# Performance work log

Measured on AMD Instinct MI355X. Metric: run time of the kernel, lower is better.

## Reference

```python
import jax, jax.numpy as jnp
import numpy as np

B, L, W = 4096, 30, 5          # batch, MAX_TOKEN_LENGTH, WINDOW_SIZE
A, E = 30, 128                 # ALPHABET_SIZE, embedding dim
C = 40                         # OUT_CHANNELS
H, T = 128, 3                  # LSTM_UNITS, num CRF tags
LIN = W * C                    # 200
EPS = 1e-5


def setup_inputs():
    key = jax.random.key(0)
    ks = jax.random.split(key, 24)
    def rn(k, shape, s=0.1):
        return jax.random.normal(k, shape, jnp.float32) * s
    return {
        'x': jax.random.randint(ks[0], (B, L, W), 0, A, jnp.int32),
        'emb': rn(ks[1], (A, E), 1.0),
        'conv_w': rn(ks[2], (C, E, 3)),
        'conv_b': rn(ks[3], (C,)),
        'bn1_g': 1.0 + rn(ks[4], (C,)),
        'bn1_b': rn(ks[5], (C,)),
        'bn1_m': rn(ks[6], (C,)),
        'bn1_v': 0.5 + jax.random.uniform(ks[7], (C,), jnp.float32),
        'w_ih_f': rn(ks[8], (4 * H, LIN)),
        'w_hh_f': rn(ks[9], (4 * H, H)),
        'b_f': rn(ks[10], (4 * H,)),
        'w_ih_b': rn(ks[11], (4 * H, LIN)),
        'w_hh_b': rn(ks[12], (4 * H, H)),
        'b_b': rn(ks[13], (4 * H,)),
        'bn2_g': 1.0 + rn(ks[14], (2 * H,)),
        'bn2_b': rn(ks[15], (2 * H,)),
        'bn2_m': rn(ks[16], (2 * H,)),
        'bn2_v': 0.5 + jax.random.uniform(ks[17], (2 * H,), jnp.float32),
        'fc_w': rn(ks[18], (T, 2 * H)),
        'fc_b': rn(ks[19], (T,)),
        'trans': rn(ks[20], (T, T)),
        'start_t': rn(ks[21], (T,)),
        'end_t': rn(ks[22], (T,)),
    }


def _lstm_dir(seq, w_ih, w_hh, b, reverse):
    # seq: [B, L, F]; torch gate order i, f, g, o
    xs = jnp.einsum('blf,gf->lbg', seq, w_ih) + b  # [L, B, 4H]
    h0 = jnp.zeros((seq.shape[0], H), seq.dtype)
    def step(carry, xt):
        h, c = carry
        z = xt + h @ w_hh.T
        i, f, g, o = jnp.split(z, 4, axis=-1)
        c = jax.nn.sigmoid(f) * c + jax.nn.sigmoid(i) * jnp.tanh(g)
        h = jax.nn.sigmoid(o) * jnp.tanh(c)
        return (h, c), h
    _, hs = jax.lax.scan(step, (h0, h0), xs, reverse=reverse)
    return hs.transpose(1, 0, 2)  # [B, L, H]


def _viterbi(emis, mask, trans, start_t, end_t):
    # emis: [B, L, T], mask: [B, L] bool
    score = start_t + emis[:, 0]                      # [B, T]
    def step(score, inp):
        e_t, m_t = inp                                # [B, T], [B]
        cand = score[:, :, None] + trans              # [B, Tprev, Tnext]
        ptr = jnp.argmax(cand, axis=1)                # [B, T]
        new = jnp.max(cand, axis=1) + e_t
        return jnp.where(m_t[:, None], new, score), ptr
    score, hist = jax.lax.scan(
        step, score, (emis[:, 1:].transpose(1, 0, 2), mask[:, 1:].T))
    score = score + end_t
    best = jnp.max(score, axis=1)                     # [B] path scores
    last = jnp.argmax(score, axis=1)                  # [B]
    def back(tag, inp):
        h_t, m_t = inp
        prev = jnp.take_along_axis(h_t, tag[:, None], axis=1)[:, 0]
        tag = jnp.where(m_t, prev, tag)
        return tag, tag
    _, ys = jax.lax.scan(back, last, (hist, mask[:, 1:].T), reverse=True)
    tags = jnp.concatenate([ys, last[None]], axis=0).T  # [B, L]
    return best, tags


def reference(x, emb, conv_w, conv_b, bn1_g, bn1_b, bn1_m, bn1_v,
              w_ih_f, w_hh_f, b_f, w_ih_b, w_hh_b, b_b,
              bn2_g, bn2_b, bn2_m, bn2_v, fc_w, fc_b, trans, start_t, end_t):
    mask = x[:, :, 2] > 0                             # [B, L]
    e = emb[x.reshape(B * L, W)]                      # [N, W, E]  (dropout=eval noop)
    e = e.transpose(0, 2, 1)                          # [N, E, W]
    y = jax.lax.conv_general_dilated(
        e, conv_w, (1,), [(1, 1)],
        dimension_numbers=('NCH', 'OIH', 'NCH')) + conv_b[:, None]
    # BatchNorm1d (inference, running stats)
    y = (y - bn1_m[:, None]) * (bn1_g / jnp.sqrt(bn1_v + EPS))[:, None] + bn1_b[:, None]
    y = jax.nn.relu(y)
    # MaxPool1d(k=3, stride=1, pad=1): length preserved
    y = jax.lax.reduce_window(y, -jnp.inf, jax.lax.max,
                              (1, 1, 3), (1, 1, 1),
                              [(0, 0), (0, 0), (1, 1)])
    y = y.reshape(B, L, LIN)                          # torch.flatten is channel-major = row-major reshape
    hf = _lstm_dir(y, w_ih_f, w_hh_f, b_f, False)
    hb = _lstm_dir(y, w_ih_b, w_hh_b, b_b, True)
    h = jnp.concatenate([hf, hb], axis=-1)            # [B, L, 2H]
    h = (h - bn2_m) * (bn2_g / jnp.sqrt(bn2_v + EPS)) + bn2_b
    emis = h @ fc_w.T + fc_b                          # [B, L, T]
    return _viterbi(emis, mask, trans, start_t, end_t)
```

## Files before the change

kernel.cpp:

```cpp
#include <hip/hip_runtime.h>
#include <math.h>

#define BB    4096
#define LL    30
#define WW    5
#define CC    40
#define HH    128
#define TT    3
#define KA    328
#define NB    32
#define NT_   512
#define FSTR  232
#define HSTR  136
#define CW    1056

#define WS_P    0
#define WS_BC   3600
#define WS_BG   3648
#define WS_WFC  4672
#define WS_EB   5440
#define WS_WBF  5504
#define WS_EMIS (5504 + 540672)

typedef __bf16 bf16x8 __attribute__((ext_vector_type(8)));
typedef float  f32x4  __attribute__((ext_vector_type(4)));
typedef unsigned short u16x8 __attribute__((ext_vector_type(8)));

__device__ __forceinline__ float sigm(float x) {
    return __builtin_amdgcn_rcpf(1.0f + __expf(-x));
}
__device__ __forceinline__ float tanh_fast(float x) {
    return 2.0f * __builtin_amdgcn_rcpf(1.0f + __expf(-2.0f * x)) - 1.0f;
}
__device__ __forceinline__ unsigned short f2bf(float f) {
    unsigned u = __builtin_bit_cast(unsigned, f);
    return (unsigned short)((u + 0x7FFFu + ((u >> 16) & 1u)) >> 16);
}
__device__ __forceinline__ float bf2f(unsigned short h) {
    unsigned u = ((unsigned)h) << 16;
    return __builtin_bit_cast(float, u);
}

__global__ void prep_kernel(const float* __restrict__ emb, const float* __restrict__ conv_w,
                            const float* __restrict__ conv_b,
                            const float* __restrict__ bn1_g, const float* __restrict__ bn1_b,
                            const float* __restrict__ bn1_m, const float* __restrict__ bn1_v,
                            const float* __restrict__ w_ih_f, const float* __restrict__ w_hh_f,
                            const float* __restrict__ b_f,
                            const float* __restrict__ w_ih_b, const float* __restrict__ w_hh_b,
                            const float* __restrict__ b_b,
                            const float* __restrict__ bn2_g, const float* __restrict__ bn2_b,
                            const float* __restrict__ bn2_m, const float* __restrict__ bn2_v,
                            const float* __restrict__ fc_w, const float* __restrict__ fc_b,
                            float* __restrict__ ws)
{
    const int gid = blockIdx.x * blockDim.x + threadIdx.x;
    const int gsz = gridDim.x * blockDim.x;

    for (int idx = gid; idx < 3600; idx += gsz) {
        int k = idx / 1200, rem = idx % 1200, a = rem / 40, c = rem % 40;
        float s1 = bn1_g[c] / sqrtf(bn1_v[c] + 1e-5f);
        float acc = 0.f;
        for (int e = 0; e < 128; ++e)
            acc += emb[a * 128 + e] * conv_w[(c * 128 + e) * 3 + k];
        ws[WS_P + idx] = acc * s1;
    }
    for (int c = gid; c < CC; c += gsz) {
        float s1 = bn1_g[c] / sqrtf(bn1_v[c] + 1e-5f);
        ws[WS_BC + c] = (conv_b[c] - bn1_m[c]) * s1 + bn1_b[c];
    }
    for (int i = gid; i < 1024; i += gsz) {
        int d = i >> 9, g = i & 511;
        ws[WS_BG + i] = d ? b_b[g] : b_f[g];
    }
    for (int i = gid; i < 768; i += gsz) {
        int d = i / 384, r = i % 384, t = r / 128, u = r % 128;
        int j = d * 128 + u;
        float s2 = bn2_g[j] / sqrtf(bn2_v[j] + 1e-5f);
        ws[WS_WFC + i] = fc_w[t * 256 + j] * s2;
    }
    for (int t = gid; t < TT; t += gsz) {
        float acc = fc_b[t];
        for (int j = 0; j < 256; ++j) {
            float s2 = bn2_g[j] / sqrtf(bn2_v[j] + 1e-5f);
            acc += fc_w[t * 256 + j] * (bn2_b[j] - bn2_m[j] * s2);
        }
        ws[WS_EB + t] = acc;
    }
    unsigned short* wsu = (unsigned short*)ws;
    for (int i = gid; i < 2 * 512 * CW; i += gsz) {
        int d = i / (512 * CW), r = i % (512 * CW);
        int n = r / CW, q = r % CW;
        int Ks = q / 96, t = q % 96, s = t / 32, k32 = t % 32;
        int k = Ks * 32 + k32;
        int u = n >> 2, g = n & 3, row = g * 128 + u;
        const float* wih = d ? w_ih_b : w_ih_f;
        const float* whh = d ? w_hh_b : w_hh_f;
        float w = (k < 200) ? wih[row * 200 + k]
                            : ((k >= 224) ? whh[row * 128 + (k - 224)] : 0.f);
        unsigned short t0 = f2bf(w);
        float r1 = w - bf2f(t0);
        unsigned short t1 = f2bf(r1);
        unsigned short t2 = f2bf(r1 - bf2f(t1));
        wsu[2 * WS_WBF + i] = (s == 0) ? t0 : ((s == 1) ? t1 : t2);
    }
}

__global__ __launch_bounds__(512, 2)
void lstm_kernel(const int* __restrict__ x, float* __restrict__ ws)
{
    __shared__ unsigned short Fh[2][NB * FSTR], Fl[2][NB * FSTR], Fm[2][NB * FSTR];
    __shared__ unsigned short Hh[2][NB * HSTR], Hl[2][NB * HSTR], Hm[2][NB * HSTR];
    __shared__ float Pp_s[3600];
    __shared__ float Wfc_s[384];
    __shared__ float biasC_s[40];

    const int tid = threadIdx.x;
    const int d   = blockIdx.x & 1;
    const int b0  = (blockIdx.x >> 1) * NB;

    const unsigned short* __restrict__ Wb =
        (const unsigned short*)ws + 2 * WS_WBF + d * (512 * CW);
    float* emis = ws + WS_EMIS + d * (BB * LL * TT);

    for (int i = tid; i < 3600; i += NT_) Pp_s[i] = ws[WS_P + i];
    for (int i = tid; i < 384;  i += NT_) Wfc_s[i] = ws[WS_WFC + d * 384 + i];
    for (int i = tid; i < 40;   i += NT_) biasC_s[i] = ws[WS_BC + i];
    for (int i = tid; i < NB * FSTR; i += NT_) {
        ((unsigned*)Fh)[i] = 0u; ((unsigned*)Fl)[i] = 0u; ((unsigned*)Fm)[i] = 0u;
    }
    for (int i = tid; i < NB * HSTR; i += NT_) {
        ((unsigned*)Hh)[i] = 0u; ((unsigned*)Hl)[i] = 0u; ((unsigned*)Hm)[i] = 0u;
    }

    const int lane = tid & 63;
    const int wv   = tid >> 6;
    const int quad = lane >> 4;
    const int ml   = lane & 15;

    const unsigned short* __restrict__ Wn[4] = {
        Wb + (wv * 64 +  0 + ml) * CW + quad * 8,
        Wb + (wv * 64 + 16 + ml) * CW + quad * 8,
        Wb + (wv * 64 + 32 + ml) * CW + quad * 8,
        Wb + (wv * 64 + 48 + ml) * CW + quad * 8
    };

    const float* bgp = ws + WS_BG + d * 512;
    int   un[4];
    float bIv[4], bFv[4], bGv[4], bOv[4];
    #pragma unroll
    for (int nt = 0; nt < 4; ++nt) {
        int u = wv * 16 + nt * 4 + quad;
        un[nt]  = u;
        bIv[nt] = bgp[u];
        bFv[nt] = bgp[128 + u];
        bGv[nt] = bgp[256 + u];
        bOv[nt] = bgp[384 + u];
    }

    float cst[2][4];
    #pragma unroll
    for (int mt = 0; mt < 2; ++mt)
        #pragma unroll
        for (int nt = 0; nt < 4; ++nt) cst[mt][nt] = 0.f;

    __syncthreads();

#define FEAT_ONE(LPOS, BUF, P)                                                 \
    {                                                                          \
        int bb = (P) / CC, c = (P) % CC;                                       \
        const int* tok = x + (((b0 + bb) * LL) + (LPOS)) * WW;                 \
        int t0 = tok[0], t1 = tok[1], t2 = tok[2], t3 = tok[3], t4 = tok[4];   \
        float bc = biasC_s[c];                                                 \
        float a0 = bc + Pp_s[(30 + t0) * 40 + c] + Pp_s[(60 + t1) * 40 + c];   \
        float a1 = bc + Pp_s[t0 * 40 + c] + Pp_s[(30 + t1) * 40 + c] + Pp_s[(60 + t2) * 40 + c]; \
        float a2 = bc + Pp_s[t1 * 40 + c] + Pp_s[(30 + t2) * 40 + c] + Pp_s[(60 + t3) * 40 + c]; \
        float a3 = bc + Pp_s[t2 * 40 + c] + Pp_s[(30 + t3) * 40 + c] + Pp_s[(60 + t4) * 40 + c]; \
        float a4 = bc + Pp_s[t3 * 40 + c] + Pp_s[(30 + t4) * 40 + c];          \
        a0 = fmaxf(a0, 0.f); a1 = fmaxf(a1, 0.f); a2 = fmaxf(a2, 0.f);         \
        a3 = fmaxf(a3, 0.f); a4 = fmaxf(a4, 0.f);                              \
        float f[5];                                                            \
        f[0] = fmaxf(a0, a1);                                                  \
        f[1] = fmaxf(fmaxf(a0, a1), a2);                                       \
        f[2] = fmaxf(fmaxf(a1, a2), a3);                                       \
        f[3] = fmaxf(fmaxf(a2, a3), a4);                                       \
        f[4] = fmaxf(a3, a4);                                                  \
        int base = bb * FSTR + c * 5;                                          \
        _Pragma("unroll")                                                      \
        for (int j = 0; j < 5; ++j) {                                          \
            unsigned short h0 = f2bf(f[j]);                                    \
            float r1 = f[j] - bf2f(h0);                                        \
            unsigned short h1 = f2bf(r1);                                      \
            unsigned short h2 = f2bf(r1 - bf2f(h1));                           \
            Fh[BUF][base + j] = h0;                                            \
            Fl[BUF][base + j] = h1;                                            \
            Fm[BUF][base + j] = h2;                                            \
        }                                                                      \
    }

#define FEAT_ALL(LPOS, BUF)                                                    \
    {                                                                          \
        FEAT_ONE(LPOS, BUF, tid)                                               \
        FEAT_ONE(LPOS, BUF, tid + 512)                                         \
        if (tid >= 256) FEAT_ONE(LPOS, BUF, tid + 768)                         \
    }

#define EMIS_BODY(LPOS, HB)                                                    \
    {                                                                          \
        int bb = tid / 6, r6 = tid % 6, t = r6 >> 1, seg = r6 & 1;             \
        int hoff = bb * HSTR + seg * 64;                                       \
        const float* wfc = &Wfc_s[t * 128 + seg * 64];                         \
        float s = 0.f;                                                         \
        _Pragma("unroll")                                                      \
        for (int i = 0; i < 8; ++i) {                                          \
            u16x8 v0 = *(const u16x8*)&Hh[HB][hoff + i * 8];                   \
            u16x8 v1 = *(const u16x8*)&Hl[HB][hoff + i * 8];                   \
            u16x8 v2 = *(const u16x8*)&Hm[HB][hoff + i * 8];                   \
            _Pragma("unroll")                                                  \
            for (int j = 0; j < 8; ++j) {                                      \
                float h = bf2f(v0[j]) + bf2f(v1[j]) + bf2f(v2[j]);             \
                s += h * wfc[i * 8 + j];                                       \
            }                                                                  \
        }                                                                      \
        s += __shfl_xor(s, 1);                                                 \
        if (seg == 0)                                                          \
            emis[(((b0 + bb) * LL) + (LPOS)) * TT + t] = s;                    \
    }

    {
        const int l0 = d ? (LL - 1) : 0;
        FEAT_ALL(l0, 0)
    }

#define WLOAD(B, P, KS)                                                        \
        {                                                                      \
            B[0] = *(const bf16x8*)((P) + (KS) * 96);                          \
            B[1] = *(const bf16x8*)((P) + (KS) * 96 + 32);                     \
            B[2] = *(const bf16x8*)((P) + (KS) * 96 + 64);                     \
        }
#define LDA(BUF, KS)                                                           \
        {                                                                      \
            if ((KS) < 7) {                                                    \
                const int ko_ = (KS) * 32 + quad * 8;                          \
                ah[BUF][0] = *(const bf16x8*)&Fh[fb][ml * FSTR + ko_];         \
                al[BUF][0] = *(const bf16x8*)&Fl[fb][ml * FSTR + ko_];         \
                am[BUF][0] = *(const bf16x8*)&Fm[fb][ml * FSTR + ko_];         \
                ah[BUF][1] = *(const bf16x8*)&Fh[fb][(16 + ml) * FSTR + ko_];  \
                al[BUF][1] = *(const bf16x8*)&Fl[fb][(16 + ml) * FSTR + ko_];  \
                am[BUF][1] = *(const bf16x8*)&Fm[fb][(16 + ml) * FSTR + ko_];  \
            } else {                                                           \
                const int ko_ = ((KS) - 7) * 32 + quad * 8;                    \
                ah[BUF][0] = *(const bf16x8*)&Hh[hr][ml * HSTR + ko_];         \
                al[BUF][0] = *(const bf16x8*)&Hl[hr][ml * HSTR + ko_];         \
                am[BUF][0] = *(const bf16x8*)&Hm[hr][ml * HSTR + ko_];         \
                ah[BUF][1] = *(const bf16x8*)&Hh[hr][(16 + ml) * HSTR + ko_];  \
                al[BUF][1] = *(const bf16x8*)&Hl[hr][(16 + ml) * HSTR + ko_];  \
                am[BUF][1] = *(const bf16x8*)&Hm[hr][(16 + ml) * HSTR + ko_];  \
            }                                                                  \
        }
#define GEMM6X(B, CB, NT)                                                      \
        {                                                                      \
            acc[0][NT] = __builtin_amdgcn_mfma_f32_16x16x32_bf16(B[0], ah[CB][0], acc[0][NT], 0, 0, 0); \
            acc[0][NT] = __builtin_amdgcn_mfma_f32_16x16x32_bf16(B[0], al[CB][0], acc[0][NT], 0, 0, 0); \
            acc[0][NT] = __builtin_amdgcn_mfma_f32_16x16x32_bf16(B[1], ah[CB][0], acc[0][NT], 0, 0, 0); \
            acc[0][NT] = __builtin_amdgcn_mfma_f32_16x16x32_bf16(B[1], al[CB][0], acc[0][NT], 0, 0, 0); \
            acc[0][NT] = __builtin_amdgcn_mfma_f32_16x16x32_bf16(B[2], ah[CB][0], acc[0][NT], 0, 0, 0); \
            acc[0][NT] = __builtin_amdgcn_mfma_f32_16x16x32_bf16(B[0], am[CB][0], acc[0][NT], 0, 0, 0); \
            acc[1][NT] = __builtin_amdgcn_mfma_f32_16x16x32_bf16(B[0], ah[CB][1], acc[1][NT], 0, 0, 0); \
            acc[1][NT] = __builtin_amdgcn_mfma_f32_16x16x32_bf16(B[0], al[CB][1], acc[1][NT], 0, 0, 0); \
            acc[1][NT] = __builtin_amdgcn_mfma_f32_16x16x32_bf16(B[1], ah[CB][1], acc[1][NT], 0, 0, 0); \
            acc[1][NT] = __builtin_amdgcn_mfma_f32_16x16x32_bf16(B[1], al[CB][1], acc[1][NT], 0, 0, 0); \
            acc[1][NT] = __builtin_amdgcn_mfma_f32_16x16x32_bf16(B[2], ah[CB][1], acc[1][NT], 0, 0, 0); \
            acc[1][NT] = __builtin_amdgcn_mfma_f32_16x16x32_bf16(B[0], am[CB][1], acc[1][NT], 0, 0, 0); \
        }

    bf16x8 wX[2][3], wY[2][3];
    WLOAD(wX[0], Wn[0], 0)
    WLOAD(wX[1], Wn[1], 0)

    __syncthreads();

    for (int step = 0; step < LL; ++step) {
        const int fb = step & 1;
        const int hw = step & 1;
        const int hr = hw ^ 1;

        f32x4 acc[2][4];
        #pragma unroll
        for (int mt = 0; mt < 2; ++mt)
            #pragma unroll
            for (int nt = 0; nt < 4; ++nt)
                acc[mt][nt] = (f32x4){0.f, 0.f, 0.f, 0.f};

        {
            bf16x8 ah[2][2], al[2][2], am[2][2];
            LDA(0, 0)

            #pragma unroll
            for (int Ks = 0; Ks < 11; ++Ks) {
                const int cb = Ks & 1, nb = cb ^ 1;

                WLOAD(wY[0], Wn[2], Ks)
                WLOAD(wY[1], Wn[3], Ks)
                if (Ks < 10) LDA(nb, Ks + 1)

                __builtin_amdgcn_s_setprio(1);
                GEMM6X(wX[0], cb, 0)
                GEMM6X(wX[1], cb, 1)
                __builtin_amdgcn_s_setprio(0);

                if (Ks < 10) {
                    WLOAD(wX[0], Wn[0], Ks + 1)
                    WLOAD(wX[1], Wn[1], Ks + 1)
                }
                __builtin_amdgcn_s_setprio(1);
                GEMM6X(wY[0], cb, 2)
                GEMM6X(wY[1], cb, 3)
                __builtin_amdgcn_s_setprio(0);

                if (Ks == 4 && step + 1 < LL && (wv & 1) == 0) {
                    const int lnext = d ? (LL - 2 - step) : (step + 1);
                    FEAT_ALL(lnext, fb ^ 1)
                }
                if (Ks == 8 && step + 1 < LL && (wv & 1) == 1) {
                    const int lnext = d ? (LL - 2 - step) : (step + 1);
                    FEAT_ALL(lnext, fb ^ 1)
                }
            }
        }

        if (step > 0 && tid < 192) {
            const int lprev = d ? (LL - step) : (step - 1);
            EMIS_BODY(lprev, hr)
        }

        #pragma unroll
        for (int mt = 0; mt < 2; ++mt) {
            #pragma unroll
            for (int nt = 0; nt < 4; ++nt) {
                float zi = acc[mt][nt][0] + bIv[nt];
                float zf = acc[mt][nt][1] + bFv[nt];
                float zg = acc[mt][nt][2] + bGv[nt];
                float zo = acc[mt][nt][3] + bOv[nt];
                float cn = sigm(zf) * cst[mt][nt] + sigm(zi) * tanh_fast(zg);
                cst[mt][nt] = cn;
                float h = sigm(zo) * tanh_fast(cn);
                unsigned short h0 = f2bf(h);
                float r1 = h - bf2f(h0);
                unsigned short h1 = f2bf(r1);
                unsigned short h2 = f2bf(r1 - bf2f(h1));
                int idx = (mt * 16 + ml) * HSTR + un[nt];
                Hh[hw][idx] = h0;
                Hl[hw][idx] = h1;
                Hm[hw][idx] = h2;
            }
        }

        if (step + 1 < LL) {
            WLOAD(wX[0], Wn[0], 0)
            WLOAD(wX[1], Wn[1], 0)
        }

        __syncthreads();
    }
#undef GEMM6X
#undef LDA
#undef WLOAD

    if (tid < 192) {
        const int llast = d ? 0 : (LL - 1);
        const int hl_ = (LL - 1) & 1;
        EMIS_BODY(llast, hl_)
    }
#undef EMIS_BODY
#undef FEAT_ALL
#undef FEAT_ONE
}

__global__ void viterbi_kernel(const int* __restrict__ x, const float* __restrict__ ws,
                               const float* __restrict__ trans,
                               const float* __restrict__ start_t,
                               const float* __restrict__ end_t,
                               float* __restrict__ out)
{
    int b = blockIdx.x * blockDim.x + threadIdx.x;
    if (b >= BB) return;
    const float* eF = ws + WS_EMIS;
    const float* eB = ws + WS_EMIS + BB * LL * TT;
    const float eb0 = ws[WS_EB + 0], eb1 = ws[WS_EB + 1], eb2 = ws[WS_EB + 2];
    float tr[9];
    #pragma unroll
    for (int i = 0; i < 9; ++i) tr[i] = trans[i];

    int base = b * LL * TT;
    float s0 = start_t[0] + eF[base + 0] + eB[base + 0] + eb0;
    float s1 = start_t[1] + eF[base + 1] + eB[base + 1] + eb1;
    float s2 = start_t[2] + eF[base + 2] + eB[base + 2] + eb2;

    unsigned hist[LL - 1];
    unsigned maskbits = 0;

    #pragma unroll
    for (int l = 1; l < LL; ++l) {
        bool m = x[(b * LL + l) * WW + 2] > 0;
        if (m) maskbits |= (1u << l);
        int idx = base + l * TT;
        float e0 = eF[idx + 0] + eB[idx + 0] + eb0;
        float e1 = eF[idx + 1] + eB[idx + 1] + eb1;
        float e2 = eF[idx + 2] + eB[idx + 2] + eb2;

        float ns[3]; int pt[3];
        #pragma unroll
        for (int nt = 0; nt < 3; ++nt) {
            float c0 = s0 + tr[0 * 3 + nt];
            float c1 = s1 + tr[1 * 3 + nt];
            float c2 = s2 + tr[2 * 3 + nt];
            int p = 0; float bc = c0;
            if (c1 > bc) { bc = c1; p = 1; }
            if (c2 > bc) { bc = c2; p = 2; }
            ns[nt] = bc; pt[nt] = p;
        }
        ns[0] += e0; ns[1] += e1; ns[2] += e2;
        hist[l - 1] = (unsigned)pt[0] | ((unsigned)pt[1] << 2) | ((unsigned)pt[2] << 4);
        if (m) { s0 = ns[0]; s1 = ns[1]; s2 = ns[2]; }
    }
    s0 += end_t[0]; s1 += end_t[1]; s2 += end_t[2];
    float best = s0; int last = 0;
    if (s1 > best) { best = s1; last = 1; }
    if (s2 > best) { best = s2; last = 2; }

    out[b] = best;
    float* tags = out + BB + b * LL;
    int tag = last;
    tags[LL - 1] = (float)last;
    #pragma unroll
    for (int l = LL - 1; l >= 1; --l) {
        int prev = (int)((hist[l - 1] >> (2 * tag)) & 3u);
        if (maskbits & (1u << l)) tag = prev;
        tags[l - 1] = (float)tag;
    }
}

extern "C" void kernel_launch(void* const* d_in, const int* in_sizes, int n_in,
                              void* d_out, int out_size, void* d_ws, size_t ws_size,
                              hipStream_t stream)
{
    const int*   x      = (const int*)  d_in[0];
    const float* emb    = (const float*)d_in[1];
    const float* conv_w = (const float*)d_in[2];
    const float* conv_b = (const float*)d_in[3];
    const float* bn1_g  = (const float*)d_in[4];
    const float* bn1_b  = (const float*)d_in[5];
    const float* bn1_m  = (const float*)d_in[6];
    const float* bn1_v  = (const float*)d_in[7];
    const float* w_ih_f = (const float*)d_in[8];
    const float* w_hh_f = (const float*)d_in[9];
    const float* b_f    = (const float*)d_in[10];
    const float* w_ih_b = (const float*)d_in[11];
    const float* w_hh_b = (const float*)d_in[12];
    const float* b_b    = (const float*)d_in[13];
    const float* bn2_g  = (const float*)d_in[14];
    const float* bn2_b  = (const float*)d_in[15];
    const float* bn2_m  = (const float*)d_in[16];
    const float* bn2_v  = (const float*)d_in[17];
    const float* fc_w   = (const float*)d_in[18];
    const float* fc_b   = (const float*)d_in[19];
    const float* trans  = (const float*)d_in[20];
    const float* start_t= (const float*)d_in[21];
    const float* end_t  = (const float*)d_in[22];

    float* ws  = (float*)d_ws;
    float* out = (float*)d_out;

    prep_kernel<<<256, 256, 0, stream>>>(emb, conv_w, conv_b,
                                         bn1_g, bn1_b, bn1_m, bn1_v,
                                         w_ih_f, w_hh_f, b_f,
                                         w_ih_b, w_hh_b, b_b,
                                         bn2_g, bn2_b, bn2_m, bn2_v,
                                         fc_w, fc_b, ws);
    lstm_kernel<<<256, 512, 0, stream>>>(x, ws);
    viterbi_kernel<<<16, 256, 0, stream>>>(x, ws, trans, start_t, end_t, out);
}
```

Measured before the change: 705.8 us.

## Overlap gate epilogue with final MFMA chunk and move emission into shadow slots

Peels the last K-step of the recurrent GEMM so the gate nonlinearities for tiles 0-1 run while the MFMAs for tiles 2-3 are issued, overlapping the epilogue with matrix work. The emission dot-product moves from after the GEMM into the same mid-loop shadow slot as next-step feature generation. Which waves take the early or late slot now follows a new parity key rather than plain wave parity, and the feature work is split unevenly across threads to offset the emission load on threads below 192. This adds register pressure and changes instruction scheduling, which could cost occupancy or add stalls.

```diff
diff --git a/kernel.cpp b/kernel.cpp
--- a/kernel.cpp
+++ b/kernel.cpp
@@ -137,6 +137,7 @@
     const int wv   = tid >> 6;
     const int quad = lane >> 4;
     const int ml   = lane & 15;
+    const int skey = (wv ^ (wv >> 2)) & 1;
 
     const unsigned short* __restrict__ Wn[4] = {
         Wb + (wv * 64 +  0 + ml) * CW + quad * 8,
@@ -198,11 +199,12 @@
         }                                                                      \
     }
 
-#define FEAT_ALL(LPOS, BUF)                                                    \
+#define FEAT_ITEMS(LPOS, BUF)                                                  \
     {                                                                          \
         FEAT_ONE(LPOS, BUF, tid)                                               \
-        FEAT_ONE(LPOS, BUF, tid + 512)                                         \
-        if (tid >= 256) FEAT_ONE(LPOS, BUF, tid + 768)                         \
+        if (tid >= 192) FEAT_ONE(LPOS, BUF, tid + 320)                         \
+        if (tid >= 192) FEAT_ONE(LPOS, BUF, tid + 640)                         \
+        if (tid >= 384) FEAT_ONE(LPOS, BUF, tid + 768)                         \
     }
 
 #define EMIS_BODY(LPOS, HB)                                                    \
@@ -227,9 +229,21 @@
             emis[(((b0 + bb) * LL) + (LPOS)) * TT + t] = s;                    \
     }
 
+#define SHADOW_WORK(STEP_, FBN)                                                \
+    {                                                                          \
+        if ((STEP_) + 1 < LL) {                                                \
+            const int lnext = d ? (LL - 2 - (STEP_)) : ((STEP_) + 1);          \
+            FEAT_ITEMS(lnext, FBN)                                             \
+        }                                                                      \
+        if ((STEP_) > 0 && tid < 192) {                                        \
+            const int lprev = d ? (LL - (STEP_)) : ((STEP_) - 1);              \
+            EMIS_BODY(lprev, hr)                                               \
+        }                                                                      \
+    }
+
     {
         const int l0 = d ? (LL - 1) : 0;
-        FEAT_ALL(l0, 0)
+        FEAT_ITEMS(l0, 0)
     }
 
 #define WLOAD(B, P, KS)                                                        \
@@ -273,6 +287,25 @@
             acc[1][NT] = __builtin_amdgcn_mfma_f32_16x16x32_bf16(B[2], ah[CB][1], acc[1][NT], 0, 0, 0); \
             acc[1][NT] = __builtin_amdgcn_mfma_f32_16x16x32_bf16(B[0], am[CB][1], acc[1][NT], 0, 0, 0); \
         }
+#define GATES_NT(NT)                                                           \
+        {                                                                      \
+            _Pragma("unroll")                                                  \
+            for (int mt = 0; mt < 2; ++mt) {                                   \
+                float zi = acc[mt][NT][0] + bIv[NT];                           \
+                float zf = acc[mt][NT][1] + bFv[NT];                           \
+                float zg = acc[mt][NT][2] + bGv[NT];                           \
+                float zo = acc[mt][NT][3] + bOv[NT];                           \
+                float cn = sigm(zf) * cst[mt][NT] + sigm(zi) * tanh_fast(zg);  \
+                cst[mt][NT] = cn;                                              \
+                float h = sigm(zo) * tanh_fast(cn);                            \
+                unsigned short h0 = f2bf(h);                                   \
+                float r1 = h - bf2f(h0);                                       \
+                unsigned short h1 = f2bf(r1);                                  \
+                unsigned short h2 = f2bf(r1 - bf2f(h1));                       \
+                int idx = (mt * 16 + ml) * HSTR + un[NT];                      \
+                Hh[hw][idx] = h0; Hl[hw][idx] = h1; Hm[hw][idx] = h2;          \
+            }                                                                  \
+        }
 
     bf16x8 wX[2][3], wY[2][3];
     WLOAD(wX[0], Wn[0], 0)
@@ -297,72 +330,56 @@
             LDA(0, 0)
 
             #pragma unroll
-            for (int Ks = 0; Ks < 11; ++Ks) {
+            for (int Ks = 0; Ks < 10; ++Ks) {
                 const int cb = Ks & 1, nb = cb ^ 1;
 
                 WLOAD(wY[0], Wn[2], Ks)
                 WLOAD(wY[1], Wn[3], Ks)
-                if (Ks < 10) LDA(nb, Ks + 1)
+                LDA(nb, Ks + 1)
 
                 __builtin_amdgcn_s_setprio(1);
                 GEMM6X(wX[0], cb, 0)
                 GEMM6X(wX[1], cb, 1)
                 __builtin_amdgcn_s_setprio(0);
 
-                if (Ks < 10) {
-                    WLOAD(wX[0], Wn[0], Ks + 1)
-                    WLOAD(wX[1], Wn[1], Ks + 1)
-                }
+                WLOAD(wX[0], Wn[0], Ks + 1)
+                WLOAD(wX[1], Wn[1], Ks + 1)
                 __builtin_amdgcn_s_setprio(1);
                 GEMM6X(wY[0], cb, 2)
                 GEMM6X(wY[1], cb, 3)
                 __builtin_amdgcn_s_setprio(0);
 
-                if (Ks == 4 && step + 1 < LL && (wv & 1) == 0) {
-                    const int lnext = d ? (LL - 2 - step) : (step + 1);
-                    FEAT_ALL(lnext, fb ^ 1)
-                }
-                if (Ks == 8 && step + 1 < LL && (wv & 1) == 1) {
-                    const int lnext = d ? (LL - 2 - step) : (step + 1);
-                    FEAT_ALL(lnext, fb ^ 1)
-                }
+                if (Ks == 3 && skey == 0) SHADOW_WORK(step, fb ^ 1)
+                if (Ks == 7 && skey == 1) SHADOW_WORK(step, fb ^ 1)
             }
-        }
-
-        if (step > 0 && tid < 192) {
-            const int lprev = d ? (LL - step) : (step - 1);
-            EMIS_BODY(lprev, hr)
-        }
-
-        #pragma unroll
-        for (int mt = 0; mt < 2; ++mt) {
-            #pragma unroll
-            for (int nt = 0; nt < 4; ++nt) {
-                float zi = acc[mt][nt][0] + bIv[nt];
-                float zf = acc[mt][nt][1] + bFv[nt];
-                float zg = acc[mt][nt][2] + bGv[nt];
-                float zo = acc[mt][nt][3] + bOv[nt];
-                float cn = sigm(zf) * cst[mt][nt] + sigm(zi) * tanh_fast(zg);
-                cst[mt][nt] = cn;
-                float h = sigm(zo) * tanh_fast(cn);
-                unsigned short h0 = f2bf(h);
-                float r1 = h - bf2f(h0);
-                unsigned short h1 = f2bf(r1);
-                unsigned short h2 = f2bf(r1 - bf2f(h1));
-                int idx = (mt * 16 + ml) * HSTR + un[nt];
-                Hh[hw][idx] = h0;
-                Hl[hw][idx] = h1;
-                Hm[hw][idx] = h2;
+
+            WLOAD(wY[0], Wn[2], 10)
+            WLOAD(wY[1], Wn[3], 10)
+
+            __builtin_amdgcn_s_setprio(1);
+            GEMM6X(wX[0], 0, 0)
+            GEMM6X(wX[1], 0, 1)
+            __builtin_amdgcn_s_setprio(0);
+
+            if (step + 1 < LL) {
+                WLOAD(wX[0], Wn[0], 0)
+                WLOAD(wX[1], Wn[1], 0)
             }
-        }
-
-        if (step + 1 < LL) {
-            WLOAD(wX[0], Wn[0], 0)
-            WLOAD(wX[1], Wn[1], 0)
+            GATES_NT(0)
+            GATES_NT(1)
+
+            __builtin_amdgcn_s_setprio(1);
+            GEMM6X(wY[0], 0, 2)
+            GEMM6X(wY[1], 0, 3)
+            __builtin_amdgcn_s_setprio(0);
+
+            GATES_NT(2)
+            GATES_NT(3)
         }
 
         __syncthreads();
     }
+#undef GATES_NT
 #undef GEMM6X
 #undef LDA
 #undef WLOAD
@@ -372,8 +389,9 @@
         const int hl_ = (LL - 1) & 1;
         EMIS_BODY(llast, hl_)
     }
+#undef SHADOW_WORK
 #undef EMIS_BODY
-#undef FEAT_ALL
+#undef FEAT_ITEMS
 #undef FEAT_ONE
 }
 
```

After: 721.6 us. +2.2%, slower.
